# Kernel optimization log

Measured on AMD Instinct MI355X. Metric: run time of the kernel, lower is better.

## Reference

```python
import jax, jax.numpy as jnp
import numpy as np

B = 65536


def conv1d(x, w, b=None, stride=1, pad=0):
    # x: [B, C_in, L], w: [C_out, C_in, K]
    y = jax.lax.conv_general_dilated(x, w, (stride,), [(pad, pad)],
                                     dimension_numbers=('NCH', 'OIH', 'NCH'))
    if b is not None:
        y = y + b[None, :, None]
    return y


def setup_inputs() -> dict:
    key = jax.random.key(0)
    ks = jax.random.split(key, 17)
    s = 0.05
    return {
        'data': jax.random.normal(ks[0], (B, 512), jnp.float32),
        'sr': 16000,
        'stft_w': jax.random.normal(ks[1], (258, 1, 256), jnp.float32) * s,
        'e1_w': jax.random.normal(ks[2], (128, 129, 3), jnp.float32) * s,
        'e1_b': jax.random.normal(ks[3], (128,), jnp.float32) * s,
        'e2_w': jax.random.normal(ks[4], (64, 128, 3), jnp.float32) * s,
        'e2_b': jax.random.normal(ks[5], (64,), jnp.float32) * s,
        'e3_w': jax.random.normal(ks[6], (64, 64, 3), jnp.float32) * s,
        'e3_b': jax.random.normal(ks[7], (64,), jnp.float32) * s,
        'e4_w': jax.random.normal(ks[8], (128, 64, 3), jnp.float32) * s,
        'e4_b': jax.random.normal(ks[9], (128,), jnp.float32) * s,
        'w_ih': jax.random.normal(ks[10], (512, 128), jnp.float32) * s,
        'w_hh': jax.random.normal(ks[11], (512, 128), jnp.float32) * s,
        'b_ih': jax.random.normal(ks[12], (512,), jnp.float32) * s,
        'b_hh': jax.random.normal(ks[13], (512,), jnp.float32) * s,
        'dec_w': jax.random.normal(ks[14], (1, 128, 1), jnp.float32) * s,
        'dec_b': jax.random.normal(ks[15], (1,), jnp.float32) * s,
    }


def reference(data, sr, stft_w, e1_w, e1_b, e2_w, e2_b, e3_w, e3_b,
              e4_w, e4_b, w_ih, w_hh, b_ih, b_hh, dec_w, dec_b):
    # First streaming call: zero context, zero LSTM state.
    context_size = 64 if sr == 16000 else 32
    b = data.shape[0]
    ctx = jnp.zeros((b, context_size), data.dtype)
    x = jnp.concatenate([ctx, data], axis=1)          # [B, 576]
    # --- STFT: reflect-pad right by 64, strided conv ---
    x = jnp.pad(x, ((0, 0), (0, 64)), mode='reflect')[:, None, :]  # [B,1,640]
    spec = conv1d(x, stft_w, None, stride=128)         # [B,258,4]
    real = spec[:, :129, :6]
    imag = spec[:, 129:, :6]
    mag = jnp.sqrt(real * real + imag * imag)          # [B,129,4]
    # --- encoder: 4 conv1d + relu blocks ---
    x = jax.nn.relu(conv1d(mag, e1_w, e1_b, 1, 1))     # [B,128,4]
    x = jax.nn.relu(conv1d(x, e2_w, e2_b, 2, 1))       # [B,64,2]
    x = jax.nn.relu(conv1d(x, e3_w, e3_b, 2, 1))       # [B,64,1]
    x = jax.nn.relu(conv1d(x, e4_w, e4_b, 1, 1))       # [B,128,1]
    # --- decoder: LSTMCell (zero initial state) ---
    xt = x[:, :, 0]                                    # squeeze(-1): [B,128]
    h0 = jnp.zeros((b, 128), xt.dtype)
    c0 = jnp.zeros((b, 128), xt.dtype)
    gates = xt @ w_ih.T + b_ih + h0 @ w_hh.T + b_hh    # [B,512]
    i, f, g, o = jnp.split(gates, 4, axis=1)           # torch gate order i,f,g,o
    c = jax.nn.sigmoid(f) * c0 + jax.nn.sigmoid(i) * jnp.tanh(g)
    h = jax.nn.sigmoid(o) * jnp.tanh(c)
    # Dropout is identity in eval mode; then relu, 1x1 conv, sigmoid.
    y = jax.nn.relu(h)[:, :, None]                     # [B,128,1]
    y = jax.nn.sigmoid(conv1d(y, dec_w, dec_b, 1, 0))  # [B,1,1]
    return y
```

## Files before the change

kernel.cpp:

```cpp
#include <hip/hip_runtime.h>


typedef unsigned short u16;
typedef unsigned int u32;
typedef __attribute__((ext_vector_type(8))) short bf16x8;
typedef __attribute__((ext_vector_type(4))) float f32x4;

__device__ __forceinline__ float bf2f(u16 u) {
    return __uint_as_float(((u32)u) << 16);
}
__device__ __forceinline__ u16 f2bf(float f) {
    u32 x = __float_as_uint(f);
    return (u16)((x + 0x7fffu + ((x >> 16) & 1u)) >> 16);
}
__device__ __forceinline__ float sigm(float x) {
    return 1.0f / (1.0f + __expf(-x));
}
__device__ __forceinline__ float tanh_f(float x) {
    float e = __expf(2.0f * x);
    return 1.0f - 2.0f / (e + 1.0f);
}
__device__ __forceinline__ float ldany(const void* p, int idx, int fp32) {
    if (fp32) return ((const float*)p)[idx];
    return bf2f(((const u16*)p)[idx]);
}
__device__ __forceinline__ bf16x8 as_h(uint4 v) {
    union { uint4 u; bf16x8 h; } x; x.u = v; return x.h;
}
#define MFMA(A_, B_, C_) __builtin_amdgcn_mfma_f32_16x16x32_bf16((A_), (B_), (C_), 0, 0, 0)

#define O_WST  0
#define O_W1   34816
#define O_W2   61440
#define O_W3   74752
#define O_W4   78848
#define O_WIH  82944
#define O_B1   115712
#define O_B2   115840
#define O_B3   115904
#define O_B4   115968
#define O_BIH  116096
#define O_DECW 116608
#define O_DECB 116736
#define O_FLAG 116737
#define NCVT   116737

__global__ __launch_bounds__(256) void vad_detect(const void* __restrict__ stft,
                                                  float* __restrict__ dst) {
    if (threadIdx.x == 0 && blockIdx.x == 0) {
        const u16* p = (const u16*)stft;
        int huge = 0;
        for (int i = 0; i < 32; i++) {
            float v = bf2f(p[i]);
            if (!(v == v) || fabsf(v) > 1.0e4f) huge = 1;
        }
        dst[O_FLAG] = huge ? 1.0f : 0.0f;
    }
}

__global__ __launch_bounds__(256) void SileroVAD_83829171683562_kernel(
    void* __restrict__ out, int n, const float* __restrict__ flagp) {
    int i = blockIdx.x * 256 + threadIdx.x;
    int fp32 = (flagp[O_FLAG] != 0.0f);
    if (i < n) {
        if (fp32) ((float*)out)[i] = 0.25f;
        else      ((u16*)out)[i]   = 0x3E80;
    }
}

__device__ __forceinline__ u16 wq_stft(const void* s, int fp32, int j, int k) {
    if (j >= 258) return 0;
    int o = (j >> 1) + (j & 1) * 129;
    return f2bf(ldany(s, o * 256 + k, fp32));
}
__device__ __forceinline__ u16 wq_e1(const void* s, int fp32, int j, int k) {
    if (k >= 408) return 0;
    int tap = k / 136, f = k - tap * 136;
    if (f >= 129) return 0;
    return f2bf(ldany(s, (j * 129 + f) * 3 + tap, fp32));
}
__device__ __forceinline__ u16 wq_e2(const void* s, int fp32, int j, int k) {
    if (k >= 408) return 0;
    int tap = k / 136, c = k - tap * 136;
    if (c >= 128) return 0;
    return f2bf(ldany(s, (j * 128 + c) * 3 + tap, fp32));
}

__global__ __launch_bounds__(256) void vad_cvt_w(
    const void* __restrict__ stft, const void* __restrict__ e1w,
    const void* __restrict__ e1b,  const void* __restrict__ e2w,
    const void* __restrict__ e2b,  const void* __restrict__ e3w,
    const void* __restrict__ e3b,  const void* __restrict__ e4w,
    const void* __restrict__ e4b,  const void* __restrict__ wih,
    const void* __restrict__ bih,  const void* __restrict__ bhh,
    const void* __restrict__ decw, const void* __restrict__ decb,
    float* __restrict__ dst)
{
    int i = blockIdx.x * 256 + threadIdx.x;
    if (i >= NCVT) return;
    int fp32 = (dst[O_FLAG] != 0.0f);
    u32* D = (u32*)dst;
    if (i < O_W1) {
        int t = i * 2, j = t >> 8, k = t & 255;
        D[i] = (u32)wq_stft(stft, fp32, j, k) | ((u32)wq_stft(stft, fp32, j, k + 1) << 16);
    } else if (i < O_W2) {
        int t = (i - O_W1) * 2, j = t / 416, k = t - j * 416;
        D[i] = (u32)wq_e1(e1w, fp32, j, k) | ((u32)wq_e1(e1w, fp32, j, k + 1) << 16);
    } else if (i < O_W3) {
        int t = (i - O_W2) * 2, j = t / 416, k = t - j * 416;
        D[i] = (u32)wq_e2(e2w, fp32, j, k) | ((u32)wq_e2(e2w, fp32, j, k + 1) << 16);
    } else if (i < O_W4) {
        int t = (i - O_W3) * 2, j = t >> 7, c0 = (t & 127) >> 1;
        u16 lo = f2bf(ldany(e3w, (j * 64 + c0) * 3 + 1, fp32));
        u16 hi = f2bf(ldany(e3w, (j * 64 + c0) * 3 + 2, fp32));
        D[i] = (u32)lo | ((u32)hi << 16);
    } else if (i < O_WIH) {
        int t = (i - O_W4) * 2, j = t >> 6, k = t & 63;
        u16 lo = f2bf(ldany(e4w, (j * 64 + k) * 3 + 1, fp32));
        u16 hi = f2bf(ldany(e4w, (j * 64 + k + 1) * 3 + 1, fp32));
        D[i] = (u32)lo | ((u32)hi << 16);
    } else if (i < O_B1) {
        int t = (i - O_WIH) * 2;
        u16 lo = f2bf(ldany(wih, t, fp32));
        u16 hi = f2bf(ldany(wih, t + 1, fp32));
        D[i] = (u32)lo | ((u32)hi << 16);
    } else if (i < O_B2)  dst[i] = ldany(e1b, i - O_B1, fp32);
    else if (i < O_B3)    dst[i] = ldany(e2b, i - O_B2, fp32);
    else if (i < O_B4)    dst[i] = ldany(e3b, i - O_B3, fp32);
    else if (i < O_BIH)   dst[i] = ldany(e4b, i - O_B4, fp32);
    else if (i < O_DECW) { int j = i - O_BIH; dst[i] = ldany(bih, j, fp32) + ldany(bhh, j, fp32); }
    else if (i < O_DECB)  dst[i] = ldany(decw, i - O_DECW, fp32);
    else                  dst[i] = ldany(decb, 0, fp32);
}

__device__ __forceinline__ uint4 load_x8(const void* data, int fp32, int e, int p0) {
    uint4 v;
    if (p0 < 64) { v.x = v.y = v.z = v.w = 0u; return v; }
    if (p0 < 576) {
        if (!fp32)
            return *(const uint4*)((const u16*)data + (size_t)e * 512u + (unsigned)(p0 - 64));
        const float* s = (const float*)data + (size_t)e * 512u + (unsigned)(p0 - 64);
        v.x = (u32)f2bf(s[0]) | ((u32)f2bf(s[1]) << 16);
        v.y = (u32)f2bf(s[2]) | ((u32)f2bf(s[3]) << 16);
        v.z = (u32)f2bf(s[4]) | ((u32)f2bf(s[5]) << 16);
        v.w = (u32)f2bf(s[6]) | ((u32)f2bf(s[7]) << 16);
        return v;
    }
    u16 t[8];
    #pragma unroll
    for (int b = 0; b < 8; b++) {
        int d = 1086 - (p0 + b);
        t[b] = fp32 ? f2bf(((const float*)data)[(size_t)e * 512u + d])
                    : ((const u16*)data)[(size_t)e * 512u + d];
    }
    v.x = (u32)t[0] | ((u32)t[1] << 16);
    v.y = (u32)t[2] | ((u32)t[3] << 16);
    v.z = (u32)t[4] | ((u32)t[5] << 16);
    v.w = (u32)t[6] | ((u32)t[7] << 16);
    return v;
}

#define EB 16
__global__ __launch_bounds__(256, 3) void vad_fused(const void* __restrict__ data,
                                                    const float* __restrict__ W,
                                                    void* __restrict__ out)
{
    __shared__ __align__(16) char smem[48400];
    u16*   XH    = (u16*)smem;
    u16*   OUT1  = (u16*)smem;
    u16*   MAGE1 = (u16*)(smem + 22272);
    u16*   OUT2  = (u16*)(smem + 22272);
    u16*   OUT3  = (u16*)(smem + 30592);
    u16*   OUT4  = (u16*)(smem + 32896);
    float* REDU  = (float*)(smem + 37248);

    const int tid  = threadIdx.x;
    const int w    = __builtin_amdgcn_readfirstlane(tid >> 6);
    const int l    = tid & 63;
    const int l15  = l & 15;
    const int lg   = l >> 4;
    const int b0   = blockIdx.x * EB;
    const int fp32 = (W[O_FLAG] != 0.0f);

    #pragma unroll
    for (int it = 0; it < 5; it++) {
        int tau = tid + it * 256;
        int ridx = tau >> 4, c8 = tau & 15;
        int e = ridx / 5, h = ridx - e * 5;
        uint4 v = load_x8(data, fp32, b0 + e, h * 128 + c8 * 8);
        *(uint4*)(XH + e * 680 + h * 136 + c8 * 8) = v;
    }
    for (int i = tid; i < 2176; i += 256) {
        int e = i / 136, k = i - e * 136;
        int off = (k < 68) ? k : (k - 68 + 340);
        ((u32*)(MAGE1 + e * 816))[off] = 0u;
    }
    for (int i = tid; i < 448; i += 256) {
        int e = i / 28, r = i - e * 28;
        MAGE1[e * 816 + (r / 7 + 1) * 136 + 129 + (r % 7)] = 0;
    }
    if (tid < 8) MAGE1[16 * 816 + tid] = 0;
    __syncthreads();

    {
        const u16* WB = (const u16*)(W + O_WST);
        const u16* xb0 = XH + (l15 >> 2) * 680 + (l15 & 3) * 136 + lg * 8;
        #pragma unroll 1
        for (int q = 0; q < 5; q++) {
            if (q == 4 && w != 3) break;
            int nt = (q < 4) ? (w * 4 + q) : 16;
            const u16* bp = WB + (nt * 16 + l15) * 256 + lg * 8;
            f32x4 a0 = {0.f,0.f,0.f,0.f}, a1 = {0.f,0.f,0.f,0.f};
            f32x4 a2 = {0.f,0.f,0.f,0.f}, a3 = {0.f,0.f,0.f,0.f};
            uint4 b_0 = *(const uint4*)(bp);
            uint4 b_1 = *(const uint4*)(bp + 32);
            uint4 b_2 = *(const uint4*)(bp + 64);
            uint4 b_3 = *(const uint4*)(bp + 96);
            #pragma unroll 1
            for (int kk = 0; kk < 8; kk++) {
                int kn = (kk < 4) ? (kk + 4) : 7;
                uint4 bn = *(const uint4*)(bp + kn * 32);
                int ao = (kk >> 2) * 136 + (kk & 3) * 32;
                bf16x8 bh = as_h(b_0);
                a0 = MFMA(as_h(*(const uint4*)(xb0 + ao)),        bh, a0);
                a1 = MFMA(as_h(*(const uint4*)(xb0 + 2720 + ao)), bh, a1);
                a2 = MFMA(as_h(*(const uint4*)(xb0 + 5440 + ao)), bh, a2);
                a3 = MFMA(as_h(*(const uint4*)(xb0 + 8160 + ao)), bh, a3);
                b_0 = b_1; b_1 = b_2; b_2 = b_3; b_3 = bn;
            }
            int f = nt * 8 + (l15 >> 1);
            bool wr = ((l15 & 1) == 0) && (f <= 128);
#define ST1_EPI(MT, ACC) do { \
            _Pragma("unroll") \
            for (int r = 0; r < 4; r++) { \
                float v_ = ACC[r]; \
                float p_ = __shfl_xor(v_, 1); \
                float m_ = sqrtf(v_ * v_ + p_ * p_); \
                if (wr) MAGE1[((MT) * 4 + lg) * 816 + (r + 1) * 136 + f] = f2bf(m_); \
            } \
        } while (0)
            ST1_EPI(0, a0); ST1_EPI(1, a1); ST1_EPI(2, a2); ST1_EPI(3, a3);
        }
    }
    __syncthreads();

    for (int i = tid; i < 1472; i += 256) {
        int e = i / 92, k = i - e * 92;
        u32* bz = (u32*)(OUT1 + e * 696);
        int off;
        if (k < 68)      off = k;
        else if (k < 84) { int z = k - 68; off = (z / 4 + 1) * 68 + 64 + (z & 3); }
        else             off = 340 + (k - 84);
        bz[off] = 0u;
    }

    {
        const u16* WB = (const u16*)(W + O_W1);
        const u16* ar0 = MAGE1 + (l15 >> 2) * 816 + (l15 & 3) * 136 + lg * 8;
        #pragma unroll 1
        for (int ji = 0; ji < 2; ji++) {
            int j = (w * 2 + ji) * 16 + l15;
            const u16* bp = WB + j * 416 + lg * 8;
            float bias = W[O_B1 + j];
            f32x4 a0 = {0.f,0.f,0.f,0.f}, a1 = {0.f,0.f,0.f,0.f};
            f32x4 a2 = {0.f,0.f,0.f,0.f}, a3 = {0.f,0.f,0.f,0.f};
            uint4 b_0 = *(const uint4*)(bp);
            uint4 b_1 = *(const uint4*)(bp + 32);
            uint4 b_2 = *(const uint4*)(bp + 64);
            uint4 b_3 = *(const uint4*)(bp + 96);
            #pragma unroll 1
            for (int kk = 0; kk < 13; kk++) {
                int kn = (kk < 9) ? (kk + 4) : 12;
                uint4 bn = *(const uint4*)(bp + kn * 32);
                int ao = kk * 32;
                bf16x8 bh = as_h(b_0);
                a0 = MFMA(as_h(*(const uint4*)(ar0 + ao)),        bh, a0);
                a1 = MFMA(as_h(*(const uint4*)(ar0 + 3264 + ao)), bh, a1);
                a2 = MFMA(as_h(*(const uint4*)(ar0 + 6528 + ao)), bh, a2);
                a3 = MFMA(as_h(*(const uint4*)(ar0 + 9792 + ao)), bh, a3);
                b_0 = b_1; b_1 = b_2; b_2 = b_3; b_3 = bn;
            }
#define ST2_EPI(MT, ACC) do { \
            _Pragma("unroll") \
            for (int r = 0; r < 4; r++) { \
                float v_ = ACC[r] + bias; \
                OUT1[((MT) * 4 + lg) * 696 + (r + 1) * 136 + j] = f2bf(v_ > 0.f ? v_ : 0.f); \
            } \
        } while (0)
            ST2_EPI(0, a0); ST2_EPI(1, a1); ST2_EPI(2, a2); ST2_EPI(3, a3);
        }
    }
    __syncthreads();

    {
        const u16* WB = (const u16*)(W + O_W2);
        int j = w * 16 + l15;
        const u16* bp = WB + j * 416 + lg * 8;
        float bias = W[O_B2 + j];
        const u16* ar0 = OUT1 + (l15 >> 1) * 696 + (l15 & 1) * 272 + lg * 8;
        f32x4 a0 = {0.f,0.f,0.f,0.f}, a1 = {0.f,0.f,0.f,0.f};
        uint4 b_0 = *(const uint4*)(bp);
        uint4 b_1 = *(const uint4*)(bp + 32);
        uint4 b_2 = *(const uint4*)(bp + 64);
        uint4 b_3 = *(const uint4*)(bp + 96);
        #pragma unroll 1
        for (int kk = 0; kk < 13; kk++) {
            int kn = (kk < 9) ? (kk + 4) : 12;
            uint4 bn = *(const uint4*)(bp + kn * 32);
            int ao = kk * 32;
            bf16x8 bh = as_h(b_0);
            a0 = MFMA(as_h(*(const uint4*)(ar0 + ao)),        bh, a0);
            a1 = MFMA(as_h(*(const uint4*)(ar0 + 5568 + ao)), bh, a1);
            b_0 = b_1; b_1 = b_2; b_2 = b_3; b_3 = bn;
        }
#define ST3_EPI(MT, ACC) do { \
        _Pragma("unroll") \
        for (int r = 0; r < 4; r++) { \
            int rg = (MT) * 16 + lg * 4 + r; \
            float v_ = ACC[r] + bias; \
            OUT2[(rg >> 1) * 260 + 2 * j + (rg & 1)] = f2bf(v_ > 0.f ? v_ : 0.f); \
        } \
    } while (0)
        ST3_EPI(0, a0); ST3_EPI(1, a1);
    }
    __syncthreads();

    {
        const u16* ap = OUT2 + l15 * 260 + lg * 8;
        const u16* WB = (const u16*)(W + O_W3);
        int j = w * 16 + l15;
        const u16* bp = WB + j * 128 + lg * 8;
        f32x4 acc = {0.f, 0.f, 0.f, 0.f};
        #pragma unroll 1
        for (int kk = 0; kk < 4; kk++)
            acc = MFMA(as_h(*(const uint4*)(ap + kk * 32)),
                       as_h(*(const uint4*)(bp + kk * 32)), acc);
        float bias = W[O_B3 + j];
        #pragma unroll
        for (int r = 0; r < 4; r++) {
            float v = acc[r] + bias;
            OUT3[(lg * 4 + r) * 72 + j] = f2bf(v > 0.f ? v : 0.f);
        }
    }
    __syncthreads();

    {
        const u16* ap = OUT3 + l15 * 72 + lg * 8;
        uint4 a0 = *(const uint4*)(ap);
        uint4 a1 = *(const uint4*)(ap + 32);
        const u16* WB = (const u16*)(W + O_W4);
        #pragma unroll 1
        for (int ni = 0; ni < 2; ni++) {
            int j = (w * 2 + ni) * 16 + l15;
            const u16* bp = WB + j * 64 + lg * 8;
            f32x4 acc = {0.f, 0.f, 0.f, 0.f};
            acc = MFMA(as_h(a0), as_h(*(const uint4*)(bp)), acc);
            acc = MFMA(as_h(a1), as_h(*(const uint4*)(bp + 32)), acc);
            float bias = W[O_B4 + j];
            #pragma unroll
            for (int r = 0; r < 4; r++) {
                float v = acc[r] + bias;
                OUT4[(lg * 4 + r) * 136 + j] = f2bf(v > 0.f ? v : 0.f);
            }
        }
    }
    __syncthreads();

    {
        const u16* ap = OUT4 + l15 * 136 + lg * 8;
        const u16* WB = (const u16*)(W + O_WIH);
        float part[4] = {0.f, 0.f, 0.f, 0.f};
        #pragma unroll 1
        for (int ni = 0; ni < 2; ni++) {
            int c = (w * 2 + ni) * 16 + l15;
            const u16* bi = WB + c * 128 + lg * 8;
            f32x4 gi = {0.f,0.f,0.f,0.f}, gg = {0.f,0.f,0.f,0.f}, go = {0.f,0.f,0.f,0.f};
            uint4 Bi = *(const uint4*)(bi);
            uint4 Bg = *(const uint4*)(bi + 32768);
            uint4 Bo = *(const uint4*)(bi + 49152);
            #pragma unroll 1
            for (int kk = 0; kk < 4; kk++) {
                int kn = (kk < 3) ? (kk + 1) : 3;
                uint4 Ni = *(const uint4*)(bi + kn * 32);
                uint4 Ng = *(const uint4*)(bi + 32768 + kn * 32);
                uint4 No = *(const uint4*)(bi + 49152 + kn * 32);
                bf16x8 av = as_h(*(const uint4*)(ap + kk * 32));
                gi = MFMA(av, as_h(Bi), gi);
                gg = MFMA(av, as_h(Bg), gg);
                go = MFMA(av, as_h(Bo), go);
                Bi = Ni; Bg = Ng; Bo = No;
            }
            float bI = W[O_BIH + c], bG = W[O_BIH + 256 + c], bO = W[O_BIH + 384 + c];
            float dw = W[O_DECW + c];
            #pragma unroll
            for (int r = 0; r < 4; r++) {
                float cs = sigm(gi[r] + bI) * tanh_f(gg[r] + bG);
                float h  = sigm(go[r] + bO) * tanh_f(cs);
                h = h > 0.f ? h : 0.f;
                part[r] = fmaf(dw, h, part[r]);
            }
        }
        #pragma unroll
        for (int mk = 1; mk < 16; mk <<= 1) {
            #pragma unroll
            for (int r = 0; r < 4; r++) part[r] += __shfl_xor(part[r], mk);
        }
        if (l15 == 0) {
            #pragma unroll
            for (int r = 0; r < 4; r++) REDU[w * 16 + lg * 4 + r] = part[r];
        }
    }
    __syncthreads();

    if (tid < 16) {
        float s = REDU[tid] + REDU[16 + tid] + REDU[32 + tid] + REDU[48 + tid];
        float y = sigm(s + W[O_DECB]);
        if (fp32) ((float*)out)[b0 + tid] = y;
        else      ((u16*)out)[b0 + tid]   = f2bf(y);
    }
}

extern "C" void kernel_launch(void* const* d_in, const int* in_sizes, int n_in,
                              void* d_out, int out_size, void* d_ws, size_t ws_size,
                              hipStream_t stream) {
    (void)in_sizes; (void)n_in; (void)ws_size;
    float* Wf = (float*)d_ws;

    vad_detect<<<1, 64, 0, stream>>>(d_in[2], Wf);

    SileroVAD_83829171683562_kernel<<<(out_size + 255) / 256, 256, 0, stream>>>(
        d_out, out_size, Wf);

    vad_cvt_w<<<(NCVT + 255) / 256, 256, 0, stream>>>(
        d_in[2],  d_in[3],  d_in[4],  d_in[5],  d_in[6],  d_in[7],
        d_in[8],  d_in[9],  d_in[10], d_in[11], d_in[13], d_in[14],
        d_in[15], d_in[16], Wf);

    vad_fused<<<65536 / EB, 256, 0, stream>>>(d_in[0], Wf, d_out);
}
```

Before: 491.9 us.

## Double fused VAD block to 512 threads and split per-stage work across eight waves

The fused kernel now launches 512 threads (eight waves) per block instead of 256, keeping 16 batch elements per block. Each stage is repartitioned so every wave handles fewer output tiles: STFT, e1, e4 and LSTM columns per wave are halved, and e2 is split by row half. The final reduction now sums eight partial sums. The aim is more resident waves per CU under the same LDS footprint, which should hide latency better and shorten the serial per-wave loops. In exchange, the e3 stage idles half the waves, and the tighter launch bound (512, 6) may force register limits or spills.

```diff
diff --git a/kernel.cpp b/kernel.cpp
--- a/kernel.cpp
+++ b/kernel.cpp
@@ -161,7 +161,7 @@
 }
 
 #define EB 16
-__global__ __launch_bounds__(256, 3) void vad_fused(const void* __restrict__ data,
+__global__ __launch_bounds__(512, 6) void vad_fused(const void* __restrict__ data,
                                                     const float* __restrict__ W,
                                                     void* __restrict__ out)
 {
@@ -182,20 +182,18 @@
     const int b0   = blockIdx.x * EB;
     const int fp32 = (W[O_FLAG] != 0.0f);
 
-    #pragma unroll
-    for (int it = 0; it < 5; it++) {
-        int tau = tid + it * 256;
+    for (int tau = tid; tau < 1280; tau += 512) {
         int ridx = tau >> 4, c8 = tau & 15;
         int e = ridx / 5, h = ridx - e * 5;
         uint4 v = load_x8(data, fp32, b0 + e, h * 128 + c8 * 8);
         *(uint4*)(XH + e * 680 + h * 136 + c8 * 8) = v;
     }
-    for (int i = tid; i < 2176; i += 256) {
+    for (int i = tid; i < 2176; i += 512) {
         int e = i / 136, k = i - e * 136;
         int off = (k < 68) ? k : (k - 68 + 340);
         ((u32*)(MAGE1 + e * 816))[off] = 0u;
     }
-    for (int i = tid; i < 448; i += 256) {
+    for (int i = tid; i < 448; i += 512) {
         int e = i / 28, r = i - e * 28;
         MAGE1[e * 816 + (r / 7 + 1) * 136 + 129 + (r % 7)] = 0;
     }
@@ -206,9 +204,9 @@
         const u16* WB = (const u16*)(W + O_WST);
         const u16* xb0 = XH + (l15 >> 2) * 680 + (l15 & 3) * 136 + lg * 8;
         #pragma unroll 1
-        for (int q = 0; q < 5; q++) {
-            if (q == 4 && w != 3) break;
-            int nt = (q < 4) ? (w * 4 + q) : 16;
+        for (int q = 0; q < 3; q++) {
+            if (q == 2 && w != 7) break;
+            int nt = (q < 2) ? (w * 2 + q) : 16;
             const u16* bp = WB + (nt * 16 + l15) * 256 + lg * 8;
             f32x4 a0 = {0.f,0.f,0.f,0.f}, a1 = {0.f,0.f,0.f,0.f};
             f32x4 a2 = {0.f,0.f,0.f,0.f}, a3 = {0.f,0.f,0.f,0.f};
@@ -244,7 +242,7 @@
     }
     __syncthreads();
 
-    for (int i = tid; i < 1472; i += 256) {
+    for (int i = tid; i < 1472; i += 512) {
         int e = i / 92, k = i - e * 92;
         u32* bz = (u32*)(OUT1 + e * 696);
         int off;
@@ -257,48 +255,11 @@
     {
         const u16* WB = (const u16*)(W + O_W1);
         const u16* ar0 = MAGE1 + (l15 >> 2) * 816 + (l15 & 3) * 136 + lg * 8;
-        #pragma unroll 1
-        for (int ji = 0; ji < 2; ji++) {
-            int j = (w * 2 + ji) * 16 + l15;
-            const u16* bp = WB + j * 416 + lg * 8;
-            float bias = W[O_B1 + j];
-            f32x4 a0 = {0.f,0.f,0.f,0.f}, a1 = {0.f,0.f,0.f,0.f};
-            f32x4 a2 = {0.f,0.f,0.f,0.f}, a3 = {0.f,0.f,0.f,0.f};
-            uint4 b_0 = *(const uint4*)(bp);
-            uint4 b_1 = *(const uint4*)(bp + 32);
-            uint4 b_2 = *(const uint4*)(bp + 64);
-            uint4 b_3 = *(const uint4*)(bp + 96);
-            #pragma unroll 1
-            for (int kk = 0; kk < 13; kk++) {
-                int kn = (kk < 9) ? (kk + 4) : 12;
-                uint4 bn = *(const uint4*)(bp + kn * 32);
-                int ao = kk * 32;
-                bf16x8 bh = as_h(b_0);
-                a0 = MFMA(as_h(*(const uint4*)(ar0 + ao)),        bh, a0);
-                a1 = MFMA(as_h(*(const uint4*)(ar0 + 3264 + ao)), bh, a1);
-                a2 = MFMA(as_h(*(const uint4*)(ar0 + 6528 + ao)), bh, a2);
-                a3 = MFMA(as_h(*(const uint4*)(ar0 + 9792 + ao)), bh, a3);
-                b_0 = b_1; b_1 = b_2; b_2 = b_3; b_3 = bn;
-            }
-#define ST2_EPI(MT, ACC) do { \
-            _Pragma("unroll") \
-            for (int r = 0; r < 4; r++) { \
-                float v_ = ACC[r] + bias; \
-                OUT1[((MT) * 4 + lg) * 696 + (r + 1) * 136 + j] = f2bf(v_ > 0.f ? v_ : 0.f); \
-            } \
-        } while (0)
-            ST2_EPI(0, a0); ST2_EPI(1, a1); ST2_EPI(2, a2); ST2_EPI(3, a3);
-        }
-    }
-    __syncthreads();
-
-    {
-        const u16* WB = (const u16*)(W + O_W2);
         int j = w * 16 + l15;
         const u16* bp = WB + j * 416 + lg * 8;
-        float bias = W[O_B2 + j];
-        const u16* ar0 = OUT1 + (l15 >> 1) * 696 + (l15 & 1) * 272 + lg * 8;
+        float bias = W[O_B1 + j];
         f32x4 a0 = {0.f,0.f,0.f,0.f}, a1 = {0.f,0.f,0.f,0.f};
+        f32x4 a2 = {0.f,0.f,0.f,0.f}, a3 = {0.f,0.f,0.f,0.f};
         uint4 b_0 = *(const uint4*)(bp);
         uint4 b_1 = *(const uint4*)(bp + 32);
         uint4 b_2 = *(const uint4*)(bp + 64);
@@ -310,22 +271,53 @@
             int ao = kk * 32;
             bf16x8 bh = as_h(b_0);
             a0 = MFMA(as_h(*(const uint4*)(ar0 + ao)),        bh, a0);
-            a1 = MFMA(as_h(*(const uint4*)(ar0 + 5568 + ao)), bh, a1);
+            a1 = MFMA(as_h(*(const uint4*)(ar0 + 3264 + ao)), bh, a1);
+            a2 = MFMA(as_h(*(const uint4*)(ar0 + 6528 + ao)), bh, a2);
+            a3 = MFMA(as_h(*(const uint4*)(ar0 + 9792 + ao)), bh, a3);
             b_0 = b_1; b_1 = b_2; b_2 = b_3; b_3 = bn;
         }
-#define ST3_EPI(MT, ACC) do { \
+#define ST2_EPI(MT, ACC) do { \
         _Pragma("unroll") \
         for (int r = 0; r < 4; r++) { \
-            int rg = (MT) * 16 + lg * 4 + r; \
             float v_ = ACC[r] + bias; \
-            OUT2[(rg >> 1) * 260 + 2 * j + (rg & 1)] = f2bf(v_ > 0.f ? v_ : 0.f); \
+            OUT1[((MT) * 4 + lg) * 696 + (r + 1) * 136 + j] = f2bf(v_ > 0.f ? v_ : 0.f); \
         } \
     } while (0)
-        ST3_EPI(0, a0); ST3_EPI(1, a1);
+        ST2_EPI(0, a0); ST2_EPI(1, a1); ST2_EPI(2, a2); ST2_EPI(3, a3);
     }
     __syncthreads();
 
     {
+        const u16* WB = (const u16*)(W + O_W2);
+        int jt = w >> 1, mh = w & 1;
+        int j = jt * 16 + l15;
+        const u16* bp = WB + j * 416 + lg * 8;
+        float bias = W[O_B2 + j];
+        const u16* ar0 = OUT1 + (l15 >> 1) * 696 + (l15 & 1) * 272 + lg * 8
+                              + mh * 5568;
+        f32x4 a0 = {0.f,0.f,0.f,0.f};
+        uint4 b_0 = *(const uint4*)(bp);
+        uint4 b_1 = *(const uint4*)(bp + 32);
+        uint4 b_2 = *(const uint4*)(bp + 64);
+        uint4 b_3 = *(const uint4*)(bp + 96);
+        #pragma unroll 1
+        for (int kk = 0; kk < 13; kk++) {
+            int kn = (kk < 9) ? (kk + 4) : 12;
+            uint4 bn = *(const uint4*)(bp + kn * 32);
+            bf16x8 bh = as_h(b_0);
+            a0 = MFMA(as_h(*(const uint4*)(ar0 + kk * 32)), bh, a0);
+            b_0 = b_1; b_1 = b_2; b_2 = b_3; b_3 = bn;
+        }
+        #pragma unroll
+        for (int r = 0; r < 4; r++) {
+            int rg = mh * 16 + lg * 4 + r;
+            float v_ = a0[r] + bias;
+            OUT2[(rg >> 1) * 260 + 2 * j + (rg & 1)] = f2bf(v_ > 0.f ? v_ : 0.f);
+        }
+    }
+    __syncthreads();
+
+    if (w < 4) {
         const u16* ap = OUT2 + l15 * 260 + lg * 8;
         const u16* WB = (const u16*)(W + O_W3);
         int j = w * 16 + l15;
@@ -349,19 +341,16 @@
         uint4 a0 = *(const uint4*)(ap);
         uint4 a1 = *(const uint4*)(ap + 32);
         const u16* WB = (const u16*)(W + O_W4);
-        #pragma unroll 1
-        for (int ni = 0; ni < 2; ni++) {
-            int j = (w * 2 + ni) * 16 + l15;
-            const u16* bp = WB + j * 64 + lg * 8;
-            f32x4 acc = {0.f, 0.f, 0.f, 0.f};
-            acc = MFMA(as_h(a0), as_h(*(const uint4*)(bp)), acc);
-            acc = MFMA(as_h(a1), as_h(*(const uint4*)(bp + 32)), acc);
-            float bias = W[O_B4 + j];
-            #pragma unroll
-            for (int r = 0; r < 4; r++) {
-                float v = acc[r] + bias;
-                OUT4[(lg * 4 + r) * 136 + j] = f2bf(v > 0.f ? v : 0.f);
-            }
+        int j = w * 16 + l15;
+        const u16* bp = WB + j * 64 + lg * 8;
+        f32x4 acc = {0.f, 0.f, 0.f, 0.f};
+        acc = MFMA(as_h(a0), as_h(*(const uint4*)(bp)), acc);
+        acc = MFMA(as_h(a1), as_h(*(const uint4*)(bp + 32)), acc);
+        float bias = W[O_B4 + j];
+        #pragma unroll
+        for (int r = 0; r < 4; r++) {
+            float v = acc[r] + bias;
+            OUT4[(lg * 4 + r) * 136 + j] = f2bf(v > 0.f ? v : 0.f);
         }
     }
     __syncthreads();
@@ -369,36 +358,33 @@
     {
         const u16* ap = OUT4 + l15 * 136 + lg * 8;
         const u16* WB = (const u16*)(W + O_WIH);
-        float part[4] = {0.f, 0.f, 0.f, 0.f};
+        int c = w * 16 + l15;
+        const u16* bi = WB + c * 128 + lg * 8;
+        f32x4 gi = {0.f,0.f,0.f,0.f}, gg = {0.f,0.f,0.f,0.f}, go = {0.f,0.f,0.f,0.f};
+        uint4 Bi = *(const uint4*)(bi);
+        uint4 Bg = *(const uint4*)(bi + 32768);
+        uint4 Bo = *(const uint4*)(bi + 49152);
         #pragma unroll 1
-        for (int ni = 0; ni < 2; ni++) {
-            int c = (w * 2 + ni) * 16 + l15;
-            const u16* bi = WB + c * 128 + lg * 8;
-            f32x4 gi = {0.f,0.f,0.f,0.f}, gg = {0.f,0.f,0.f,0.f}, go = {0.f,0.f,0.f,0.f};
-            uint4 Bi = *(const uint4*)(bi);
-            uint4 Bg = *(const uint4*)(bi + 32768);
-            uint4 Bo = *(const uint4*)(bi + 49152);
-            #pragma unroll 1
-            for (int kk = 0; kk < 4; kk++) {
-                int kn = (kk < 3) ? (kk + 1) : 3;
-                uint4 Ni = *(const uint4*)(bi + kn * 32);
-                uint4 Ng = *(const uint4*)(bi + 32768 + kn * 32);
-                uint4 No = *(const uint4*)(bi + 49152 + kn * 32);
-                bf16x8 av = as_h(*(const uint4*)(ap + kk * 32));
-                gi = MFMA(av, as_h(Bi), gi);
-                gg = MFMA(av, as_h(Bg), gg);
-                go = MFMA(av, as_h(Bo), go);
-                Bi = Ni; Bg = Ng; Bo = No;
-            }
-            float bI = W[O_BIH + c], bG = W[O_BIH + 256 + c], bO = W[O_BIH + 384 + c];
-            float dw = W[O_DECW + c];
-            #pragma unroll
-            for (int r = 0; r < 4; r++) {
-                float cs = sigm(gi[r] + bI) * tanh_f(gg[r] + bG);
-                float h  = sigm(go[r] + bO) * tanh_f(cs);
-                h = h > 0.f ? h : 0.f;
-                part[r] = fmaf(dw, h, part[r]);
-            }
+        for (int kk = 0; kk < 4; kk++) {
+            int kn = (kk < 3) ? (kk + 1) : 3;
+            uint4 Ni = *(const uint4*)(bi + kn * 32);
+            uint4 Ng = *(const uint4*)(bi + 32768 + kn * 32);
+            uint4 No = *(const uint4*)(bi + 49152 + kn * 32);
+            bf16x8 av = as_h(*(const uint4*)(ap + kk * 32));
+            gi = MFMA(av, as_h(Bi), gi);
+            gg = MFMA(av, as_h(Bg), gg);
+            go = MFMA(av, as_h(Bo), go);
+            Bi = Ni; Bg = Ng; Bo = No;
+        }
+        float bI = W[O_BIH + c], bG = W[O_BIH + 256 + c], bO = W[O_BIH + 384 + c];
+        float dw = W[O_DECW + c];
+        float part[4];
+        #pragma unroll
+        for (int r = 0; r < 4; r++) {
+            float cs = sigm(gi[r] + bI) * tanh_f(gg[r] + bG);
+            float h  = sigm(go[r] + bO) * tanh_f(cs);
+            h = h > 0.f ? h : 0.f;
+            part[r] = dw * h;
         }
         #pragma unroll
         for (int mk = 1; mk < 16; mk <<= 1) {
@@ -413,7 +399,9 @@
     __syncthreads();
 
     if (tid < 16) {
-        float s = REDU[tid] + REDU[16 + tid] + REDU[32 + tid] + REDU[48 + tid];
+        float s = 0.f;
+        #pragma unroll
+        for (int ww = 0; ww < 8; ww++) s += REDU[ww * 16 + tid];
         float y = sigm(s + W[O_DECB]);
         if (fp32) ((float*)out)[b0 + tid] = y;
         else      ((u16*)out)[b0 + tid]   = f2bf(y);
@@ -436,5 +424,5 @@
         d_in[8],  d_in[9],  d_in[10], d_in[11], d_in[13], d_in[14],
         d_in[15], d_in[16], Wf);
 
-    vad_fused<<<65536 / EB, 256, 0, stream>>>(d_in[0], Wf, d_out);
-}
+    vad_fused<<<65536 / EB, 512, 0, stream>>>(d_in[0], Wf, d_out);
+}
```

Result: faster. 448.8 us (-8.8%).
